# Performance work log

Measured on AMD Instinct MI355X. Metric: run time of the kernel, lower is better.

## Reference

```python
import jax, jax.numpy as jnp
import numpy as np

N_NODES = 50000
N_EDGES = 600000
IN_DIM = 512
HIDDEN = 128
OUT_DIM = 64
N_LAYERS = 3
EPS = 0.1


def setup_inputs() -> dict:
    key = jax.random.key(0)
    ks = jax.random.split(key, 8)
    x = jax.random.normal(ks[0], (N_NODES, IN_DIM), jnp.float32)
    edge_index = jax.random.randint(ks[1], (2, N_EDGES), 0, N_NODES, jnp.int32)
    # xavier-normal-ish scaled weights
    t1_w = jax.random.normal(ks[2], (HIDDEN, IN_DIM), jnp.float32) * (1.414 * (2.0 / (IN_DIM + HIDDEN)) ** 0.5)
    t1_b = jnp.zeros((HIDDEN,), jnp.float32)
    t2_w = jax.random.normal(ks[3], (OUT_DIM, HIDDEN), jnp.float32) * (1.414 * (2.0 / (HIDDEN + OUT_DIM)) ** 0.5)
    t2_b = jnp.zeros((OUT_DIM,), jnp.float32)
    # per-layer FAConv attention vectors: Linear(hidden, 1, bias=False)
    att_l = jax.random.normal(ks[4], (N_LAYERS, HIDDEN), jnp.float32) * 0.1
    att_r = jax.random.normal(ks[5], (N_LAYERS, HIDDEN), jnp.float32) * 0.1
    return dict(x=x, edge_index=edge_index, t1_w=t1_w, t1_b=t1_b,
                t2_w=t2_w, t2_b=t2_b, att_l=att_l, att_r=att_r)


def _gcn_norm(src, dst, n):
    # symmetric gcn_norm without self-loops (as FAConv uses): deg over targets
    deg = jax.ops.segment_sum(jnp.ones(src.shape, jnp.float32), dst, num_segments=n)
    dinv = jnp.where(deg > 0, 1.0 / jnp.sqrt(jnp.maximum(deg, 1.0)), 0.0)
    return dinv[src] * dinv[dst]  # [E]


def _fa_conv(h, raw, src, dst, al_w, ar_w, norm, n):
    # alpha = tanh(att_l . x_j + att_r . x_i), message = x_j * alpha * norm
    al = h @ al_w  # [N]
    ar = h @ ar_w  # [N]
    alpha = jnp.tanh(al[src] + ar[dst])  # [E]
    msg = h[src] * (alpha * norm)[:, None]  # [E, HIDDEN]
    out = jax.ops.segment_sum(msg, dst, num_segments=n)
    return out + EPS * raw


def reference(x, edge_index, t1_w, t1_b, t2_w, t2_b, att_l, att_r):
    src, dst = edge_index[0], edge_index[1]
    n = x.shape[0]
    norm = _gcn_norm(src, dst, n)
    h = jax.nn.relu(x @ t1_w.T + t1_b)  # dropout is identity in eval mode
    raw = h
    for i in range(N_LAYERS):
        h = _fa_conv(h, raw, src, dst, att_l[i], att_r[i], norm, n)
    emb = h @ t2_w.T + t2_b
    out = jax.nn.log_softmax(emb, axis=1)
    return out, emb
```

## Files before the change

### kernel.cpp

```cpp
#include <hip/hip_runtime.h>
#include <hip/hip_bf16.h>
#include <stdint.h>

#define NN 50000
#define NE 600000
#define IN_DIM 512
#define HID 128
#define ODIM 64
#define EPSV 0.1f
#define NBLK ((NN + 255) / 256)

typedef __attribute__((ext_vector_type(8))) short short8;
typedef __attribute__((ext_vector_type(4))) float f32x4;

__device__ __forceinline__ ushort f2bf(float f) {
    union { float f; uint32_t i; } v; v.f = f;
    uint32_t lsb = (v.i >> 16) & 1u;
    uint32_t r = v.i + 0x7fffu + lsb;
    return (ushort)(r >> 16);
}

__device__ __forceinline__ float bf2f(ushort u) {
    union { uint32_t i; float f; } v; v.i = ((uint32_t)u) << 16;
    return v.f;
}

__device__ __forceinline__ float bflo(uint32_t u) {
    union { uint32_t i; float f; } v; v.i = u << 16; return v.f;
}
__device__ __forceinline__ float bfhi(uint32_t u) {
    union { uint32_t i; float f; } v; v.i = u & 0xffff0000u; return v.f;
}

__device__ __forceinline__ short8 pack8(float4 lo, float4 hi) {
    short8 r;
    r[0] = (short)f2bf(lo.x); r[1] = (short)f2bf(lo.y);
    r[2] = (short)f2bf(lo.z); r[3] = (short)f2bf(lo.w);
    r[4] = (short)f2bf(hi.x); r[5] = (short)f2bf(hi.y);
    r[6] = (short)f2bf(hi.z); r[7] = (short)f2bf(hi.w);
    return r;
}

__device__ __forceinline__ float fast_tanh(float z) {
    z = fminf(fmaxf(z, -15.f), 15.f);
    float t = __expf(2.f * z);
    return __fdividef(t - 1.f, t + 1.f);
}

__global__ __launch_bounds__(256) void deg_kernel(const int* __restrict__ dst, int* __restrict__ deg) {
    int e = blockIdx.x * 256 + threadIdx.x;
    if (e < NE) atomicAdd(&deg[dst[e]], 1);
}

__global__ __launch_bounds__(256) void scanA_kernel(const int* __restrict__ deg,
                                                    int* __restrict__ localScan,
                                                    int* __restrict__ blockSums,
                                                    float* __restrict__ dinv) {
    __shared__ int tmp[256];
    int t = threadIdx.x;
    int i = blockIdx.x * 256 + t;
    int v = (i < NN) ? deg[i] : 0;
    tmp[t] = v;
    __syncthreads();
    for (int off = 1; off < 256; off <<= 1) {
        int add = (t >= off) ? tmp[t - off] : 0;
        __syncthreads();
        tmp[t] += add;
        __syncthreads();
    }
    if (i < NN) {
        localScan[i] = tmp[t] - v;
        dinv[i] = (v > 0) ? (1.0f / sqrtf((float)v)) : 0.0f;
    }
    if (t == 255) blockSums[blockIdx.x] = tmp[255];
}

__global__ __launch_bounds__(256) void scanB_kernel(const int* __restrict__ blockSums,
                                                    int* __restrict__ blockOff) {
    __shared__ int tmp[256];
    int t = threadIdx.x;
    int v = (t < NBLK) ? blockSums[t] : 0;
    tmp[t] = v;
    __syncthreads();
    for (int off = 1; off < 256; off <<= 1) {
        int add = (t >= off) ? tmp[t - off] : 0;
        __syncthreads();
        tmp[t] += add;
        __syncthreads();
    }
    blockOff[t] = tmp[t] - v;
}

__global__ __launch_bounds__(256) void scanC_kernel(const int* __restrict__ localScan,
                                                    const int* __restrict__ blockOff,
                                                    int* __restrict__ rowptr,
                                                    int* __restrict__ cursor) {
    int i = blockIdx.x * 256 + threadIdx.x;
    if (i < NN) {
        int v = localScan[i] + blockOff[blockIdx.x];
        rowptr[i] = v;
        cursor[i] = v;
    }
    if (i == 0) rowptr[NN] = NE;
}

__global__ __launch_bounds__(256) void fill_kernel(const int* __restrict__ src, const int* __restrict__ dst,
                                                   int* __restrict__ cursor, int* __restrict__ csr_src) {
    int e = blockIdx.x * 256 + threadIdx.x;
    if (e < NE) {
        int d = dst[e];
        int slot = atomicAdd(&cursor[d], 1);
        csr_src[slot] = src[e];
    }
}

__global__ __launch_bounds__(256) void cvtw_kernel(const float* __restrict__ w, ushort* __restrict__ wbf) {
    int i = blockIdx.x * 256 + threadIdx.x;
    if (i < HID * IN_DIM) wbf[i] = f2bf(w[i]);
}

__global__ __launch_bounds__(1024, 4) void gemm1_kernel(const float* __restrict__ x,
                                                        const ushort* __restrict__ wbf,
                                                        const float* __restrict__ b,
                                                        const float* __restrict__ attl,
                                                        const float* __restrict__ attr,
                                                        const float* __restrict__ dinv,
                                                        float* __restrict__ h,
                                                        ushort* __restrict__ hb,
                                                        float2* __restrict__ AD,
                                                        float* __restrict__ AR) {
    __shared__ __attribute__((aligned(16))) ushort b_sm[HID * IN_DIM];
    int t = threadIdx.x;
    int wv = __builtin_amdgcn_readfirstlane(t >> 6);
    int lane = t & 63;
    int m0 = blockIdx.x * 256;

    {
        uint4 bg[8];
#pragma unroll
        for (int rnd = 0; rnd < 8; ++rnd)
            bg[rnd] = *(const uint4*)(wbf + (size_t)(rnd * 1024 + t) * 8);
#pragma unroll
        for (int rnd = 0; rnd < 8; ++rnd) {
            int G = rnd * 1024 + t;
            int row = G >> 6;
            int g = G & 63;
            *(uint4*)&b_sm[(size_t)((row << 6) | (g ^ (row & 7))) * 8] = bg[rnd];
        }
    }
    __syncthreads();

    int rsel = lane & 15;
    int koff = (lane >> 4) * 8;
    int sw = rsel & 7;
    int qg = koff >> 3;
    int row = m0 + wv * 16 + rsel; if (row >= NN) row = NN - 1;
    const float* xr = x + (size_t)row * IN_DIM + koff;

    f32x4 acc[8];
#pragma unroll
    for (int tt = 0; tt < 8; ++tt) acc[tt] = (f32x4){0.f, 0.f, 0.f, 0.f};

    float4 c0lo = *(const float4*)(xr);
    float4 c0hi = *(const float4*)(xr + 4);
    float4 c1lo = *(const float4*)(xr + 32);
    float4 c1hi = *(const float4*)(xr + 36);

#pragma unroll
    for (int ks = 0; ks < 16; ks += 2) {
        float4 n0lo, n0hi, n1lo, n1hi;
        bool more = (ks + 2 < 16);
        if (more) {
            n0lo = *(const float4*)(xr + (ks + 2) * 32);
            n0hi = *(const float4*)(xr + (ks + 2) * 32 + 4);
            n1lo = *(const float4*)(xr + (ks + 3) * 32);
            n1hi = *(const float4*)(xr + (ks + 3) * 32 + 4);
        }
        short8 a0 = pack8(c0lo, c0hi);
#pragma unroll
        for (int tt = 0; tt < 8; ++tt) {
            int rb = tt * 16 + rsel;
            short8 bf = *(const short8*)&b_sm[(size_t)(rb << 9) + (size_t)(((ks * 4 + qg) ^ sw) << 3)];
            acc[tt] = __builtin_amdgcn_mfma_f32_16x16x32_bf16(a0, bf, acc[tt], 0, 0, 0);
        }
        short8 a1 = pack8(c1lo, c1hi);
#pragma unroll
        for (int tt = 0; tt < 8; ++tt) {
            int rb = tt * 16 + rsel;
            short8 bf = *(const short8*)&b_sm[(size_t)(rb << 9) + (size_t)((((ks + 1) * 4 + qg) ^ sw) << 3)];
            acc[tt] = __builtin_amdgcn_mfma_f32_16x16x32_bf16(a1, bf, acc[tt], 0, 0, 0);
        }
        if (more) { c0lo = n0lo; c0hi = n0hi; c1lo = n1lo; c1hi = n1hi; }
    }

    int rbase = (lane >> 4) * 4;
    int col0 = lane & 15;
    float alv[8], arv[8], bias[8];
#pragma unroll
    for (int tt = 0; tt < 8; ++tt) {
        alv[tt]  = attl[tt * 16 + col0];
        arv[tt]  = attr[tt * 16 + col0];
        bias[tt] = b[tt * 16 + col0];
    }
#pragma unroll
    for (int r = 0; r < 4; ++r) {
        int rrow = m0 + wv * 16 + rbase + r;
        float p = 0.f, q = 0.f;
#pragma unroll
        for (int tt = 0; tt < 8; ++tt) {
            float v = acc[tt][r] + bias[tt];
            v = v > 0.f ? v : 0.f;
            if (rrow < NN) {
                h[(size_t)rrow * HID + tt * 16 + col0] = v;
                hb[(size_t)rrow * HID + tt * 16 + col0] = f2bf(v);
            }
            p += v * alv[tt];
            q += v * arv[tt];
        }
#pragma unroll
        for (int off = 8; off; off >>= 1) { p += __shfl_xor(p, off); q += __shfl_xor(q, off); }
        if (col0 == 0 && rrow < NN) {
            float2 vv; vv.x = p; vv.y = dinv[rrow];
            AD[rrow] = vv;
            AR[rrow] = q;
        }
    }
}

__global__ __launch_bounds__(256) void agg_kernel(const ushort* __restrict__ hb,
                                                  const float* __restrict__ raw,
                                                  ushort* __restrict__ hnb,
                                                  const int* __restrict__ rowptr,
                                                  const int* __restrict__ csr_src,
                                                  const float* __restrict__ dinv,
                                                  const float2* __restrict__ AD,
                                                  const float* __restrict__ AR,
                                                  const float* __restrict__ attl_next,
                                                  const float* __restrict__ attr_next,
                                                  float2* __restrict__ ADout,
                                                  float* __restrict__ ARout) {
    int wv = __builtin_amdgcn_readfirstlane(threadIdx.x >> 6);
    int lane = threadIdx.x & 63;
    int d = blockIdx.x * 4 + wv;
    if (d >= NN) return;
    const uint32_t* h4 = (const uint32_t*)hb;
    float ar_d = AR[d];
    float dinv_d = dinv[d];
    float2 rawd = ((const float2*)raw)[(size_t)d * 64 + lane];
    float accx = EPSV * rawd.x, accy = EPSV * rawd.y;
    int e = rowptr[d], e1 = rowptr[d + 1];
    for (; e + 8 <= e1; e += 8) {
        int sv = csr_src[e + (lane & 7)];
        int s0 = __builtin_amdgcn_readfirstlane(__shfl(sv, 0));
        int s1 = __builtin_amdgcn_readfirstlane(__shfl(sv, 1));
        int s2 = __builtin_amdgcn_readfirstlane(__shfl(sv, 2));
        int s3 = __builtin_amdgcn_readfirstlane(__shfl(sv, 3));
        int s4 = __builtin_amdgcn_readfirstlane(__shfl(sv, 4));
        int s5 = __builtin_amdgcn_readfirstlane(__shfl(sv, 5));
        int s6 = __builtin_amdgcn_readfirstlane(__shfl(sv, 6));
        int s7 = __builtin_amdgcn_readfirstlane(__shfl(sv, 7));
        float2 ad0 = AD[s0], ad1 = AD[s1], ad2 = AD[s2], ad3 = AD[s3];
        float2 ad4 = AD[s4], ad5 = AD[s5], ad6 = AD[s6], ad7 = AD[s7];
        uint32_t u0 = h4[(size_t)s0 * 64 + lane];
        uint32_t u1 = h4[(size_t)s1 * 64 + lane];
        uint32_t u2 = h4[(size_t)s2 * 64 + lane];
        uint32_t u3 = h4[(size_t)s3 * 64 + lane];
        uint32_t u4 = h4[(size_t)s4 * 64 + lane];
        uint32_t u5 = h4[(size_t)s5 * 64 + lane];
        uint32_t u6 = h4[(size_t)s6 * 64 + lane];
        uint32_t u7 = h4[(size_t)s7 * 64 + lane];
        float w0 = fast_tanh(ad0.x + ar_d) * ad0.y * dinv_d;
        float w1 = fast_tanh(ad1.x + ar_d) * ad1.y * dinv_d;
        float w2 = fast_tanh(ad2.x + ar_d) * ad2.y * dinv_d;
        float w3 = fast_tanh(ad3.x + ar_d) * ad3.y * dinv_d;
        float w4 = fast_tanh(ad4.x + ar_d) * ad4.y * dinv_d;
        float w5 = fast_tanh(ad5.x + ar_d) * ad5.y * dinv_d;
        float w6 = fast_tanh(ad6.x + ar_d) * ad6.y * dinv_d;
        float w7 = fast_tanh(ad7.x + ar_d) * ad7.y * dinv_d;
        accx += w0 * bflo(u0) + w1 * bflo(u1) + w2 * bflo(u2) + w3 * bflo(u3);
        accy += w0 * bfhi(u0) + w1 * bfhi(u1) + w2 * bfhi(u2) + w3 * bfhi(u3);
        accx += w4 * bflo(u4) + w5 * bflo(u5) + w6 * bflo(u6) + w7 * bflo(u7);
        accy += w4 * bfhi(u4) + w5 * bfhi(u5) + w6 * bfhi(u6) + w7 * bfhi(u7);
    }
    for (; e + 4 <= e1; e += 4) {
        int sv = csr_src[e + (lane & 3)];
        int s0 = __builtin_amdgcn_readfirstlane(__shfl(sv, 0));
        int s1 = __builtin_amdgcn_readfirstlane(__shfl(sv, 1));
        int s2 = __builtin_amdgcn_readfirstlane(__shfl(sv, 2));
        int s3 = __builtin_amdgcn_readfirstlane(__shfl(sv, 3));
        float2 ad0 = AD[s0], ad1 = AD[s1], ad2 = AD[s2], ad3 = AD[s3];
        uint32_t u0 = h4[(size_t)s0 * 64 + lane];
        uint32_t u1 = h4[(size_t)s1 * 64 + lane];
        uint32_t u2 = h4[(size_t)s2 * 64 + lane];
        uint32_t u3 = h4[(size_t)s3 * 64 + lane];
        float w0 = fast_tanh(ad0.x + ar_d) * ad0.y * dinv_d;
        float w1 = fast_tanh(ad1.x + ar_d) * ad1.y * dinv_d;
        float w2 = fast_tanh(ad2.x + ar_d) * ad2.y * dinv_d;
        float w3 = fast_tanh(ad3.x + ar_d) * ad3.y * dinv_d;
        accx += w0 * bflo(u0) + w1 * bflo(u1) + w2 * bflo(u2) + w3 * bflo(u3);
        accy += w0 * bfhi(u0) + w1 * bfhi(u1) + w2 * bfhi(u2) + w3 * bfhi(u3);
    }
    for (; e < e1; ++e) {
        int s = __builtin_amdgcn_readfirstlane(csr_src[e]);
        float2 ad = AD[s];
        uint32_t u = h4[(size_t)s * 64 + lane];
        float w = fast_tanh(ad.x + ar_d) * ad.y * dinv_d;
        accx += w * bflo(u);
        accy += w * bfhi(u);
    }
    ((uint32_t*)hnb)[(size_t)d * 64 + lane] =
        (uint32_t)f2bf(accx) | ((uint32_t)f2bf(accy) << 16);
    if (attl_next) {
        float al0 = attl_next[2 * lane], al1 = attl_next[2 * lane + 1];
        float ar0 = attr_next[2 * lane], ar1 = attr_next[2 * lane + 1];
        float p = accx * al0 + accy * al1;
        float q = accx * ar0 + accy * ar1;
#pragma unroll
        for (int off = 32; off; off >>= 1) { p += __shfl_xor(p, off); q += __shfl_xor(q, off); }
        if (lane == 0) {
            float2 v; v.x = p; v.y = dinv_d;
            ADout[d] = v;
            ARout[d] = q;
        }
    }
}

__global__ __launch_bounds__(256) void head_kernel(const ushort* __restrict__ hb,
                                                   const float* __restrict__ w2,
                                                   const float* __restrict__ b2,
                                                   float* __restrict__ out) {
    __shared__ __attribute__((aligned(16))) ushort bhi_sm[ODIM * HID];
    __shared__ __attribute__((aligned(16))) ushort blo_sm[ODIM * HID];
    int t = threadIdx.x;
    int wv = __builtin_amdgcn_readfirstlane(t >> 6);
    int lane = t & 63;

    {
        int j = t >> 2;
        int k0 = (t & 3) * 32;
        const float* wr = w2 + (size_t)j * HID + k0;
#pragma unroll
        for (int gg = 0; gg < 4; ++gg) {
            float4 a4 = *(const float4*)(wr + gg * 8);
            float4 b4 = *(const float4*)(wr + gg * 8 + 4);
            float vals[8] = {a4.x, a4.y, a4.z, a4.w, b4.x, b4.y, b4.z, b4.w};
            short8 vhi, vlo;
#pragma unroll
            for (int e = 0; e < 8; ++e) {
                ushort hu = f2bf(vals[e]);
                ushort lu = f2bf(vals[e] - bf2f(hu));
                vhi[e] = (short)hu; vlo[e] = (short)lu;
            }
            int g = (t & 3) * 4 + gg;
            int p = g ^ (j & 7);
            *(short8*)&bhi_sm[(size_t)j * HID + p * 8] = vhi;
            *(short8*)&blo_sm[(size_t)j * HID + p * 8] = vlo;
        }
    }
    __syncthreads();

    int rsel = lane & 15;
    int q16 = lane >> 4;
    int koff = q16 * 8;
    int sw = rsel & 7;
    int m0 = blockIdx.x * 128 + wv * 32;

    f32x4 acc[2][4];
#pragma unroll
    for (int ms = 0; ms < 2; ++ms)
#pragma unroll
        for (int nt = 0; nt < 4; ++nt) acc[ms][nt] = (f32x4){0.f, 0.f, 0.f, 0.f};

#pragma unroll
    for (int ks = 0; ks < 4; ++ks) {
        short8 a[2];
#pragma unroll
        for (int ms = 0; ms < 2; ++ms) {
            int row = m0 + ms * 16 + rsel; if (row >= NN) row = NN - 1;
            a[ms] = *(const short8*)(hb + (size_t)row * HID + ks * 32 + koff);
        }
        int p = (ks * 4 + q16) ^ sw;
#pragma unroll
        for (int nt = 0; nt < 4; ++nt) {
            size_t bofs = (size_t)(nt * 16 + rsel) * HID + p * 8;
            short8 bh = *(const short8*)&bhi_sm[bofs];
            short8 bl = *(const short8*)&blo_sm[bofs];
#pragma unroll
            for (int ms = 0; ms < 2; ++ms) {
                acc[ms][nt] = __builtin_amdgcn_mfma_f32_16x16x32_bf16(a[ms], bh, acc[ms][nt], 0, 0, 0);
                acc[ms][nt] = __builtin_amdgcn_mfma_f32_16x16x32_bf16(a[ms], bl, acc[ms][nt], 0, 0, 0);
            }
        }
    }

    int col0 = lane & 15;
    float bias[4];
#pragma unroll
    for (int nt = 0; nt < 4; ++nt) bias[nt] = b2[nt * 16 + col0];
#pragma unroll
    for (int ms = 0; ms < 2; ++ms) {
#pragma unroll
        for (int r = 0; r < 4; ++r) {
            int node = m0 + ms * 16 + q16 * 4 + r;
            float v0 = acc[ms][0][r] + bias[0];
            float v1 = acc[ms][1][r] + bias[1];
            float v2 = acc[ms][2][r] + bias[2];
            float v3 = acc[ms][3][r] + bias[3];
            float m = fmaxf(fmaxf(v0, v1), fmaxf(v2, v3));
#pragma unroll
            for (int off = 8; off; off >>= 1) m = fmaxf(m, __shfl_xor(m, off));
            float s = __expf(v0 - m) + __expf(v1 - m) + __expf(v2 - m) + __expf(v3 - m);
#pragma unroll
            for (int off = 8; off; off >>= 1) s += __shfl_xor(s, off);
            float ls = m + __logf(s);
            if (node < NN) {
                out[(size_t)node * ODIM + 0 * 16 + col0] = v0 - ls;
                out[(size_t)node * ODIM + 1 * 16 + col0] = v1 - ls;
                out[(size_t)node * ODIM + 2 * 16 + col0] = v2 - ls;
                out[(size_t)node * ODIM + 3 * 16 + col0] = v3 - ls;
                size_t eb = (size_t)NN * ODIM + (size_t)node * ODIM;
                out[eb + 0 * 16 + col0] = v0;
                out[eb + 1 * 16 + col0] = v1;
                out[eb + 2 * 16 + col0] = v2;
                out[eb + 3 * 16 + col0] = v3;
            }
        }
    }
}

extern "C" void kernel_launch(void* const* d_in, const int* in_sizes, int n_in,
                              void* d_out, int out_size, void* d_ws, size_t ws_size,
                              hipStream_t stream) {
    const float* x    = (const float*)d_in[0];
    const int*   ei   = (const int*)d_in[1];
    const float* t1w  = (const float*)d_in[2];
    const float* t1b  = (const float*)d_in[3];
    const float* t2w  = (const float*)d_in[4];
    const float* t2b  = (const float*)d_in[5];
    const float* attl = (const float*)d_in[6];
    const float* attr = (const float*)d_in[7];
    float* out = (float*)d_out;

    const int* src = ei;
    const int* dst = ei + NE;

    char* ws = (char*)d_ws;
    size_t off = 0;
    auto alloc = [&](size_t bytes) { char* p = ws + off; off += (bytes + 255) & ~(size_t)255; return p; };
    float*  hA   = (float*)alloc((size_t)NN * HID * 4);
    ushort* h0b  = (ushort*)alloc((size_t)NN * HID * 2);
    ushort* h1b  = (ushort*)alloc((size_t)NN * HID * 2);
    ushort* h2b  = (ushort*)alloc((size_t)NN * HID * 2);
    ushort* h3b  = (ushort*)alloc((size_t)NN * HID * 2);
    ushort* wbf  = (ushort*)alloc((size_t)HID * IN_DIM * 2);
    int*    deg  = (int*)alloc((size_t)NN * 4);
    float*  dinv = (float*)alloc((size_t)NN * 4);
    int*    rowptr = (int*)alloc((size_t)(NN + 1) * 4);
    int*    cursor = (int*)alloc((size_t)NN * 4);
    int*    csr_src = (int*)alloc((size_t)NE * 4);
    int*    localScan = (int*)alloc((size_t)NN * 4);
    int*    blockSums = (int*)alloc((size_t)256 * 4);
    int*    blockOff  = (int*)alloc((size_t)256 * 4);
    float2* AD_A = (float2*)alloc((size_t)NN * 8);
    float*  AR_A = (float*)alloc((size_t)NN * 4);
    float2* AD_B = (float2*)alloc((size_t)NN * 8);
    float*  AR_B = (float*)alloc((size_t)NN * 4);
    (void)ws_size;

    hipMemsetAsync(deg, 0, (size_t)NN * 4, stream);

    dim3 blk(256);
    deg_kernel<<<(NE + 255) / 256, blk, 0, stream>>>(dst, deg);
    scanA_kernel<<<NBLK, blk, 0, stream>>>(deg, localScan, blockSums, dinv);
    scanB_kernel<<<1, blk, 0, stream>>>(blockSums, blockOff);
    scanC_kernel<<<NBLK, blk, 0, stream>>>(localScan, blockOff, rowptr, cursor);
    fill_kernel<<<(NE + 255) / 256, blk, 0, stream>>>(src, dst, cursor, csr_src);

    cvtw_kernel<<<(HID * IN_DIM + 255) / 256, blk, 0, stream>>>(t1w, wbf);
    gemm1_kernel<<<(NN + 255) / 256, dim3(1024), 0, stream>>>(x, wbf, t1b,
                                                              attl + 0 * HID, attr + 0 * HID,
                                                              dinv, hA, h0b, AD_A, AR_A);

    agg_kernel<<<(NN + 3) / 4, blk, 0, stream>>>(h0b, hA, h1b, rowptr, csr_src, dinv,
                                                 AD_A, AR_A, attl + 1 * HID, attr + 1 * HID, AD_B, AR_B);
    agg_kernel<<<(NN + 3) / 4, blk, 0, stream>>>(h1b, hA, h2b, rowptr, csr_src, dinv,
                                                 AD_B, AR_B, attl + 2 * HID, attr + 2 * HID, AD_A, AR_A);
    agg_kernel<<<(NN + 3) / 4, blk, 0, stream>>>(h2b, hA, h3b, rowptr, csr_src, dinv,
                                                 AD_A, AR_A, nullptr, nullptr, nullptr, nullptr);

    head_kernel<<<(NN + 127) / 128, blk, 0, stream>>>(h3b, t2w, t2b, out);
}
```

Measured before the change: 378.0 us.

## Drop fp32 hidden copy, read residual in bf16, batch edge index loads per wave

The first GEMM no longer writes an fp32 copy of the hidden features; aggregation layers read the residual term from the bf16 buffer instead. This removes a large fp32 write and three fp32 reads of the residual. The edge loop now loads up to 64 neighbour indices per wave in one coalesced load and broadcasts them with readlane, replacing per-group shuffles. The residual loses precision to bf16 rounding.

```diff
diff --git a/kernel.cpp b/kernel.cpp
--- a/kernel.cpp
+++ b/kernel.cpp
@@ -125,7 +125,6 @@
                                                         const float* __restrict__ attl,
                                                         const float* __restrict__ attr,
                                                         const float* __restrict__ dinv,
-                                                        float* __restrict__ h,
                                                         ushort* __restrict__ hb,
                                                         float2* __restrict__ AD,
                                                         float* __restrict__ AR) {
@@ -210,10 +209,7 @@
         for (int tt = 0; tt < 8; ++tt) {
             float v = acc[tt][r] + bias[tt];
             v = v > 0.f ? v : 0.f;
-            if (rrow < NN) {
-                h[(size_t)rrow * HID + tt * 16 + col0] = v;
-                hb[(size_t)rrow * HID + tt * 16 + col0] = f2bf(v);
-            }
+            if (rrow < NN) hb[(size_t)rrow * HID + tt * 16 + col0] = f2bf(v);
             p += v * alv[tt];
             q += v * arv[tt];
         }
@@ -228,7 +224,7 @@
 }
 
 __global__ __launch_bounds__(256) void agg_kernel(const ushort* __restrict__ hb,
-                                                  const float* __restrict__ raw,
+                                                  const ushort* __restrict__ rawb,
                                                   ushort* __restrict__ hnb,
                                                   const int* __restrict__ rowptr,
                                                   const int* __restrict__ csr_src,
@@ -246,67 +242,54 @@
     const uint32_t* h4 = (const uint32_t*)hb;
     float ar_d = AR[d];
     float dinv_d = dinv[d];
-    float2 rawd = ((const float2*)raw)[(size_t)d * 64 + lane];
-    float accx = EPSV * rawd.x, accy = EPSV * rawd.y;
-    int e = rowptr[d], e1 = rowptr[d + 1];
-    for (; e + 8 <= e1; e += 8) {
-        int sv = csr_src[e + (lane & 7)];
-        int s0 = __builtin_amdgcn_readfirstlane(__shfl(sv, 0));
-        int s1 = __builtin_amdgcn_readfirstlane(__shfl(sv, 1));
-        int s2 = __builtin_amdgcn_readfirstlane(__shfl(sv, 2));
-        int s3 = __builtin_amdgcn_readfirstlane(__shfl(sv, 3));
-        int s4 = __builtin_amdgcn_readfirstlane(__shfl(sv, 4));
-        int s5 = __builtin_amdgcn_readfirstlane(__shfl(sv, 5));
-        int s6 = __builtin_amdgcn_readfirstlane(__shfl(sv, 6));
-        int s7 = __builtin_amdgcn_readfirstlane(__shfl(sv, 7));
-        float2 ad0 = AD[s0], ad1 = AD[s1], ad2 = AD[s2], ad3 = AD[s3];
-        float2 ad4 = AD[s4], ad5 = AD[s5], ad6 = AD[s6], ad7 = AD[s7];
-        uint32_t u0 = h4[(size_t)s0 * 64 + lane];
-        uint32_t u1 = h4[(size_t)s1 * 64 + lane];
-        uint32_t u2 = h4[(size_t)s2 * 64 + lane];
-        uint32_t u3 = h4[(size_t)s3 * 64 + lane];
-        uint32_t u4 = h4[(size_t)s4 * 64 + lane];
-        uint32_t u5 = h4[(size_t)s5 * 64 + lane];
-        uint32_t u6 = h4[(size_t)s6 * 64 + lane];
-        uint32_t u7 = h4[(size_t)s7 * 64 + lane];
-        float w0 = fast_tanh(ad0.x + ar_d) * ad0.y * dinv_d;
-        float w1 = fast_tanh(ad1.x + ar_d) * ad1.y * dinv_d;
-        float w2 = fast_tanh(ad2.x + ar_d) * ad2.y * dinv_d;
-        float w3 = fast_tanh(ad3.x + ar_d) * ad3.y * dinv_d;
-        float w4 = fast_tanh(ad4.x + ar_d) * ad4.y * dinv_d;
-        float w5 = fast_tanh(ad5.x + ar_d) * ad5.y * dinv_d;
-        float w6 = fast_tanh(ad6.x + ar_d) * ad6.y * dinv_d;
-        float w7 = fast_tanh(ad7.x + ar_d) * ad7.y * dinv_d;
-        accx += w0 * bflo(u0) + w1 * bflo(u1) + w2 * bflo(u2) + w3 * bflo(u3);
-        accy += w0 * bfhi(u0) + w1 * bfhi(u1) + w2 * bfhi(u2) + w3 * bfhi(u3);
-        accx += w4 * bflo(u4) + w5 * bflo(u5) + w6 * bflo(u6) + w7 * bflo(u7);
-        accy += w4 * bfhi(u4) + w5 * bfhi(u5) + w6 * bfhi(u6) + w7 * bfhi(u7);
-    }
-    for (; e + 4 <= e1; e += 4) {
-        int sv = csr_src[e + (lane & 3)];
-        int s0 = __builtin_amdgcn_readfirstlane(__shfl(sv, 0));
-        int s1 = __builtin_amdgcn_readfirstlane(__shfl(sv, 1));
-        int s2 = __builtin_amdgcn_readfirstlane(__shfl(sv, 2));
-        int s3 = __builtin_amdgcn_readfirstlane(__shfl(sv, 3));
-        float2 ad0 = AD[s0], ad1 = AD[s1], ad2 = AD[s2], ad3 = AD[s3];
-        uint32_t u0 = h4[(size_t)s0 * 64 + lane];
-        uint32_t u1 = h4[(size_t)s1 * 64 + lane];
-        uint32_t u2 = h4[(size_t)s2 * 64 + lane];
-        uint32_t u3 = h4[(size_t)s3 * 64 + lane];
-        float w0 = fast_tanh(ad0.x + ar_d) * ad0.y * dinv_d;
-        float w1 = fast_tanh(ad1.x + ar_d) * ad1.y * dinv_d;
-        float w2 = fast_tanh(ad2.x + ar_d) * ad2.y * dinv_d;
-        float w3 = fast_tanh(ad3.x + ar_d) * ad3.y * dinv_d;
-        accx += w0 * bflo(u0) + w1 * bflo(u1) + w2 * bflo(u2) + w3 * bflo(u3);
-        accy += w0 * bfhi(u0) + w1 * bfhi(u1) + w2 * bfhi(u2) + w3 * bfhi(u3);
-    }
-    for (; e < e1; ++e) {
-        int s = __builtin_amdgcn_readfirstlane(csr_src[e]);
-        float2 ad = AD[s];
-        uint32_t u = h4[(size_t)s * 64 + lane];
-        float w = fast_tanh(ad.x + ar_d) * ad.y * dinv_d;
-        accx += w * bflo(u);
-        accy += w * bfhi(u);
+    uint32_t rawd = ((const uint32_t*)rawb)[(size_t)d * 64 + lane];
+    float accx = EPSV * bflo(rawd), accy = EPSV * bfhi(rawd);
+    int e0 = rowptr[d], e1 = rowptr[d + 1];
+    for (int base = e0; base < e1; base += 64) {
+        int cnt = e1 - base; if (cnt > 64) cnt = 64;
+        int gi = base + lane; if (gi > NE - 1) gi = NE - 1;
+        int myidx = csr_src[gi];
+        int c = 0;
+        for (; c + 8 <= cnt; c += 8) {
+            int s0 = __builtin_amdgcn_readlane(myidx, c + 0);
+            int s1 = __builtin_amdgcn_readlane(myidx, c + 1);
+            int s2 = __builtin_amdgcn_readlane(myidx, c + 2);
+            int s3 = __builtin_amdgcn_readlane(myidx, c + 3);
+            int s4 = __builtin_amdgcn_readlane(myidx, c + 4);
+            int s5 = __builtin_amdgcn_readlane(myidx, c + 5);
+            int s6 = __builtin_amdgcn_readlane(myidx, c + 6);
+            int s7 = __builtin_amdgcn_readlane(myidx, c + 7);
+            float2 ad0 = AD[s0], ad1 = AD[s1], ad2 = AD[s2], ad3 = AD[s3];
+            float2 ad4 = AD[s4], ad5 = AD[s5], ad6 = AD[s6], ad7 = AD[s7];
+            uint32_t u0 = h4[(size_t)s0 * 64 + lane];
+            uint32_t u1 = h4[(size_t)s1 * 64 + lane];
+            uint32_t u2 = h4[(size_t)s2 * 64 + lane];
+            uint32_t u3 = h4[(size_t)s3 * 64 + lane];
+            uint32_t u4 = h4[(size_t)s4 * 64 + lane];
+            uint32_t u5 = h4[(size_t)s5 * 64 + lane];
+            uint32_t u6 = h4[(size_t)s6 * 64 + lane];
+            uint32_t u7 = h4[(size_t)s7 * 64 + lane];
+            float w0 = fast_tanh(ad0.x + ar_d) * ad0.y * dinv_d;
+            float w1 = fast_tanh(ad1.x + ar_d) * ad1.y * dinv_d;
+            float w2 = fast_tanh(ad2.x + ar_d) * ad2.y * dinv_d;
+            float w3 = fast_tanh(ad3.x + ar_d) * ad3.y * dinv_d;
+            float w4 = fast_tanh(ad4.x + ar_d) * ad4.y * dinv_d;
+            float w5 = fast_tanh(ad5.x + ar_d) * ad5.y * dinv_d;
+            float w6 = fast_tanh(ad6.x + ar_d) * ad6.y * dinv_d;
+            float w7 = fast_tanh(ad7.x + ar_d) * ad7.y * dinv_d;
+            accx += w0 * bflo(u0) + w1 * bflo(u1) + w2 * bflo(u2) + w3 * bflo(u3);
+            accy += w0 * bfhi(u0) + w1 * bfhi(u1) + w2 * bfhi(u2) + w3 * bfhi(u3);
+            accx += w4 * bflo(u4) + w5 * bflo(u5) + w6 * bflo(u6) + w7 * bflo(u7);
+            accy += w4 * bfhi(u4) + w5 * bfhi(u5) + w6 * bfhi(u6) + w7 * bfhi(u7);
+        }
+        for (; c < cnt; ++c) {
+            int s = __builtin_amdgcn_readlane(myidx, c);
+            float2 ad = AD[s];
+            uint32_t u = h4[(size_t)s * 64 + lane];
+            float w = fast_tanh(ad.x + ar_d) * ad.y * dinv_d;
+            accx += w * bflo(u);
+            accy += w * bfhi(u);
+        }
     }
     ((uint32_t*)hnb)[(size_t)d * 64 + lane] =
         (uint32_t)f2bf(accx) | ((uint32_t)f2bf(accy) << 16);
@@ -447,7 +430,6 @@
     char* ws = (char*)d_ws;
     size_t off = 0;
     auto alloc = [&](size_t bytes) { char* p = ws + off; off += (bytes + 255) & ~(size_t)255; return p; };
-    float*  hA   = (float*)alloc((size_t)NN * HID * 4);
     ushort* h0b  = (ushort*)alloc((size_t)NN * HID * 2);
     ushort* h1b  = (ushort*)alloc((size_t)NN * HID * 2);
     ushort* h2b  = (ushort*)alloc((size_t)NN * HID * 2);
@@ -479,13 +461,13 @@
     cvtw_kernel<<<(HID * IN_DIM + 255) / 256, blk, 0, stream>>>(t1w, wbf);
     gemm1_kernel<<<(NN + 255) / 256, dim3(1024), 0, stream>>>(x, wbf, t1b,
                                                               attl + 0 * HID, attr + 0 * HID,
-                                                              dinv, hA, h0b, AD_A, AR_A);
-
-    agg_kernel<<<(NN + 3) / 4, blk, 0, stream>>>(h0b, hA, h1b, rowptr, csr_src, dinv,
+                                                              dinv, h0b, AD_A, AR_A);
+
+    agg_kernel<<<(NN + 3) / 4, blk, 0, stream>>>(h0b, h0b, h1b, rowptr, csr_src, dinv,
                                                  AD_A, AR_A, attl + 1 * HID, attr + 1 * HID, AD_B, AR_B);
-    agg_kernel<<<(NN + 3) / 4, blk, 0, stream>>>(h1b, hA, h2b, rowptr, csr_src, dinv,
+    agg_kernel<<<(NN + 3) / 4, blk, 0, stream>>>(h1b, h0b, h2b, rowptr, csr_src, dinv,
                                                  AD_B, AR_B, attl + 2 * HID, attr + 2 * HID, AD_A, AR_A);
-    agg_kernel<<<(NN + 3) / 4, blk, 0, stream>>>(h2b, hA, h3b, rowptr, csr_src, dinv,
+    agg_kernel<<<(NN + 3) / 4, blk, 0, stream>>>(h2b, h0b, h3b, rowptr, csr_src, dinv,
                                                  AD_A, AR_A, nullptr, nullptr, nullptr, nullptr);
 
     head_kernel<<<(NN + 127) / 128, blk, 0, stream>>>(h3b, t2w, t2b, out);
```

Result: no change. 371.9 us (-1.6%).
